# Performance work log

Measured on AMD Instinct MI355X. Metric: run time of the kernel, lower is better.

## Reference

```python
import jax, jax.numpy as jnp
import numpy as np

# Module hyperparameters (match init_kwargs)
C = 64      # in_channels
O = 256     # out_channels
K = 3       # filter_size
SUB = 2     # subsampling
SIGMA = 1.0
SCALE = 1.0 / SIGMA ** 2
EPS = 1e-8


def setup_inputs() -> dict:
    key = jax.random.key(0)
    k1, k2 = jax.random.split(key)
    x = jax.random.normal(k1, (32, C, 64, 64), dtype=jnp.float32)
    weight = jax.random.normal(k2, (O, C * K * K), dtype=jnp.float32)
    return {"x": x, "weight": weight}


def reference(x, weight):
    # Faithful to CKNLayer.forward, but expressed as a direct convolution
    # instead of materializing the im2col (unfold) tensor:
    #   unfold -> per-patch L2 norm -> (patches/norm) @ w_norm.T
    # == conv(x, w_norm) / patch_norm,   patch_norm = sqrt(conv(x^2, ones))
    B, _, H, W = x.shape
    pad = K // 2

    # F.normalize(weight, p=2, dim=1): clamp norm at 1e-12
    w_norm = weight / jnp.maximum(
        jnp.linalg.norm(weight, axis=1, keepdims=True), 1e-12
    )
    # torch unfold orders patch features as (c, kh, kw) -> reshape matches
    w4 = w_norm.reshape(O, C, K, K)

    dn = jax.lax.conv_dimension_numbers(x.shape, w4.shape, ('NCHW', 'OIHW', 'NCHW'))
    dots = jax.lax.conv_general_dilated(
        x, w4, window_strides=(1, 1), padding=[(pad, pad), (pad, pad)],
        dimension_numbers=dn)  # [B, O, H, W]

    ones_k = jnp.ones((1, C, K, K), x.dtype)
    sq = jax.lax.conv_general_dilated(
        x * x, ones_k, window_strides=(1, 1), padding=[(pad, pad), (pad, pad)],
        dimension_numbers=dn)  # [B, 1, H, W] = sum of squares per patch
    patch_norm = jnp.sqrt(jnp.maximum(sq, 0.0)) + EPS

    # Gaussian RBF on the unit sphere: exp(scale * (cos_sim - 1))
    out = jnp.exp(SCALE * (dots / patch_norm - 1.0))  # [B, O, H, W]

    # avg_pool2d(kernel=SUB, stride=SUB), H, W divisible by SUB
    out = out.reshape(B, O, H // SUB, SUB, W // SUB, SUB).mean(axis=(3, 5))
    return out
```

## Files before the change

### kernel.cpp

```cpp
#include <hip/hip_runtime.h>
#include <hip/hip_bf16.h>

typedef __attribute__((ext_vector_type(8))) short bf16x8;
typedef __attribute__((ext_vector_type(4))) float f32x4;
typedef __attribute__((ext_vector_type(16))) float f32x16;
typedef __attribute__((ext_vector_type(4))) unsigned u32x4;

__device__ __forceinline__ unsigned bfbits(float v) {
  __hip_bfloat16 h = __float2bfloat16(v);
  return (unsigned)*reinterpret_cast<unsigned short*>(&h);
}

__device__ __forceinline__ void wnorm_one(const float* __restrict__ w,
                                          ushort* __restrict__ wt,
                                          ushort* __restrict__ wt3,
                                          int o, int c) {
  float v[9];
  float ss = 0.f;
  const float* row = w + o * 576 + c * 9;
#pragma unroll
  for (int j = 0; j < 9; ++j) { v[j] = row[j]; ss += v[j] * v[j]; }
#pragma unroll
  for (int off = 32; off > 0; off >>= 1) ss += __shfl_xor(ss, off);
  const float inv = 1.0f / fmaxf(sqrtf(ss), 1e-12f);
  const int g = o >> 5, n = o & 31;
#pragma unroll
  for (int j = 0; j < 9; ++j) {
    const ushort bv = (ushort)bfbits(v[j] * inv);
    wt[o * 576 + j * 64 + c] = bv;
    const int ks = j * 4 + (c >> 4);
    wt3[((ks * 8 + g) * 32 + n) * 16 + (c & 15)] = bv;
  }
}

__global__ void wnorm_kernel(const float* __restrict__ w,
                             ushort* __restrict__ wt,
                             ushort* __restrict__ wt3) {
  wnorm_one(w, wt, wt3, blockIdx.x, threadIdx.x);
}

__global__ __launch_bounds__(256, 8) void xprep_kernel(
    const float* __restrict__ x, ushort* __restrict__ xt,
    float* __restrict__ css, const float* __restrict__ w,
    ushort* __restrict__ wt, ushort* __restrict__ wt3) {
  __shared__ __align__(16) unsigned tile[64 * 33];
  __shared__ __align__(16) float cssp[4 * 64];
  const int t = threadIdx.x;
  if (blockIdx.y == 32) {
    wnorm_one(w, wt, wt3, blockIdx.x * 4 + (t >> 6), t & 63);
    return;
  }
  const int y = blockIdx.x, b = blockIdx.y;
  const int c = t >> 2, m = t & 3;
  const int lane = t & 63, wv = t >> 6;

  const float* src = x + (((size_t)b * 64 + c) * 64 + y) * 64 + m * 4;
  float f[16];
#pragma unroll
  for (int j4 = 0; j4 < 4; ++j4) {
    const f32x4 v = *(const f32x4*)(src + j4 * 16);
#pragma unroll
    for (int k = 0; k < 4; ++k) f[j4 * 4 + k] = v[k];
  }
  float s[16];
#pragma unroll
  for (int j = 0; j < 16; ++j) {
    float v = f[j] * f[j];
    v += __shfl_xor(v, 4);
    v += __shfl_xor(v, 8);
    v += __shfl_xor(v, 16);
    v += __shfl_xor(v, 32);
    s[j] = v;
  }
  if (lane < 4) {
#pragma unroll
    for (int j4 = 0; j4 < 4; ++j4) {
      f32x4 v = {s[j4 * 4], s[j4 * 4 + 1], s[j4 * 4 + 2], s[j4 * 4 + 3]};
      *(f32x4*)(cssp + wv * 64 + j4 * 16 + lane * 4) = v;
    }
  }
  const int parity = c & 1;
  const int c2 = c >> 1;
#pragma unroll
  for (int j = 0; j < 16; ++j) {
    const float pf = __shfl_xor(f[j], 4);
    const bool mine = parity ? (j >= 8) : (j < 8);
    if (mine) {
      const unsigned dw = parity ? (bfbits(pf) | (bfbits(f[j]) << 16))
                                 : (bfbits(f[j]) | (bfbits(pf) << 16));
      const int px = (j >> 2) * 16 + m * 4 + (j & 3);
      tile[px * 33 + c2] = dw;
    }
  }
  __syncthreads();
  {
    const int xr = t >> 2, q = t & 3;
    unsigned d[8];
#pragma unroll
    for (int i = 0; i < 8; ++i) d[i] = tile[xr * 33 + q * 8 + i];
    ushort* dst = xt + (((size_t)b * 64 + y) * 64 + xr) * 64 + q * 16;
    u32x4 v0 = {d[0], d[1], d[2], d[3]};
    u32x4 v1 = {d[4], d[5], d[6], d[7]};
    *(u32x4*)dst = v0;
    *(u32x4*)(dst + 8) = v1;
  }
  if (t < 64) {
    const float sum = cssp[t] + cssp[64 + t] + cssp[128 + t] + cssp[192 + t];
    css[((size_t)b * 64 + y) * 64 + t] = sum;
  }
}

__global__ __launch_bounds__(512, 4) void ckn_main(
    const ushort* __restrict__ xt, const float* __restrict__ css,
    const ushort* __restrict__ wt3, float* __restrict__ out) {
  __shared__ __align__(16) char smem[67328];
  char* const xs = smem;
  float* const pool = (float*)(smem + 33792);
  float* const invp = (float*)(smem + 66816);
  const int PS = 258;

  const int tid = threadIdx.x;
  const int y0 = blockIdx.x;
  const int b = blockIdx.y;

  if (tid < 128) {
    const int ry = tid >> 6, xx = tid & 63;
    const int yc = 2 * y0 + ry;
    float s = 0.f;
#pragma unroll
    for (int dy = -1; dy <= 1; ++dy) {
      const int yy = yc + dy;
      if ((unsigned)yy < 64u) s += css[((size_t)b * 64 + yy) * 64 + xx];
    }
    const float sl = __shfl_up(s, 1);
    const float sr = __shfl_down(s, 1);
    const float tot = s + ((xx > 0) ? sl : 0.f) + ((xx < 63) ? sr : 0.f);
    invp[tid] = 1.0f / (sqrtf(fmaxf(tot, 0.f)) + 1e-8f);
  }

  if (tid < 64) {
    const int r4 = tid >> 4, colsel = (tid >> 3) & 1, cblk = tid & 7;
    *(f32x4*)(xs + r4 * 8448 + colsel * 65 * 128 + cblk * 16) =
        (f32x4){0.f, 0.f, 0.f, 0.f};
  }

  {
    const int xx = tid >> 3;
    const int c0 = 8 * ((tid & 7) ^ ((xx + 1) & 7));
    const ushort* srcb = xt + ((size_t)b * 64) * 4096 + (size_t)xx * 64 + c0;
#pragma unroll
    for (int r4 = 0; r4 < 4; ++r4) {
      const int y_img = 2 * y0 - 1 + r4;
      char* dst = xs + r4 * 8448 + 128 + tid * 16;
      if ((unsigned)y_img < 64u) {
        const ushort* src = srcb + (size_t)y_img * 4096;
        __builtin_amdgcn_global_load_lds(
            (const __attribute__((address_space(1))) void*)src,
            (__attribute__((address_space(3))) void*)dst, 16, 0, 0);
      } else {
        *(f32x4*)dst = (f32x4){0.f, 0.f, 0.f, 0.f};
      }
    }
  }

  const int lane = tid & 63;
  const int wid = tid >> 6;
  const int wave_m = wid & 1;
  const int wave_n = wid >> 1;
  const int lane31 = lane & 31;
  const int hi = lane >> 5;

  const ushort* wb3 = wt3 + (size_t)lane31 * 16 + hi * 8;
  const int g0 = wave_n * 2;

  bf16x8 bq[2][2];
#pragma unroll
  for (int nf = 0; nf < 2; ++nf) {
    bq[0][nf] = *(const bf16x8*)(wb3 + (size_t)(0 * 8 + g0 + nf) * 512);
    bq[1][nf] = *(const bf16x8*)(wb3 + (size_t)(1 * 8 + g0 + nf) * 512);
  }

  const int hi16 = hi << 4;
  int PH[2][3];
#pragma unroll
  for (int mf = 0; mf < 2; ++mf)
#pragma unroll
    for (int kw = 0; kw < 3; ++kw) {
      const int col = mf * 32 + lane31 + kw;
      PH[mf][kw] = (col * 128 + ((col & 7) << 4)) ^ hi16;
    }
  const int rb0 = wave_m * 8448;

  __syncthreads();

  f32x16 acc[2][2];
#pragma unroll
  for (int i = 0; i < 2; ++i)
#pragma unroll
    for (int j = 0; j < 2; ++j)
#pragma unroll
      for (int e = 0; e < 16; ++e) acc[i][j][e] = 0.f;

#pragma unroll
  for (int ks = 0; ks < 36; ++ks) {
    const int t9 = ks >> 2;
    const int kh = t9 / 3, kw = t9 % 3;
    const int ksc = (ks & 3) << 5;
    const int cur = ks & 1;
    bf16x8 afrag[2];
#pragma unroll
    for (int mf = 0; mf < 2; ++mf)
      afrag[mf] = *(const bf16x8*)(xs + rb0 + kh * 8448 + (PH[mf][kw] ^ ksc));
    __builtin_amdgcn_s_setprio(1);
#pragma unroll
    for (int mf = 0; mf < 2; ++mf)
#pragma unroll
      for (int nf = 0; nf < 2; ++nf)
        acc[mf][nf] = __builtin_amdgcn_mfma_f32_32x32x16_bf16(
            afrag[mf], bq[cur][nf], acc[mf][nf], 0, 0, 0);
    __builtin_amdgcn_s_setprio(0);
    if (ks + 2 < 36) {
#pragma unroll
      for (int nf = 0; nf < 2; ++nf)
        bq[cur][nf] =
            *(const bf16x8*)(wb3 + (size_t)((ks + 2) * 8 + g0 + nf) * 512);
    }
  }

  if (wave_m == 1) {
#pragma unroll
    for (int mf = 0; mf < 2; ++mf)
#pragma unroll
      for (int q = 0; q < 4; ++q) {
        const f32x4 ip = *(const f32x4*)(invp + 64 + mf * 32 + 8 * q + 4 * hi);
        const int px = mf * 16 + 4 * q + 2 * hi;
#pragma unroll
        for (int nf = 0; nf < 2; ++nf) {
          const int o = wave_n * 64 + nf * 32 + lane31;
          const float e0 = __expf(acc[mf][nf][4 * q + 0] * ip[0] - 1.f);
          const float e1 = __expf(acc[mf][nf][4 * q + 1] * ip[1] - 1.f);
          const float e2 = __expf(acc[mf][nf][4 * q + 2] * ip[2] - 1.f);
          const float e3 = __expf(acc[mf][nf][4 * q + 3] * ip[3] - 1.f);
          pool[px * PS + o] = e0 + e1;
          pool[(px + 1) * PS + o] = e2 + e3;
        }
      }
  }
  __syncthreads();
  if (wave_m == 0) {
#pragma unroll
    for (int mf = 0; mf < 2; ++mf)
#pragma unroll
      for (int q = 0; q < 4; ++q) {
        const f32x4 ip = *(const f32x4*)(invp + mf * 32 + 8 * q + 4 * hi);
        const int px = mf * 16 + 4 * q + 2 * hi;
#pragma unroll
        for (int nf = 0; nf < 2; ++nf) {
          const int o = wave_n * 64 + nf * 32 + lane31;
          const float e0 = __expf(acc[mf][nf][4 * q + 0] * ip[0] - 1.f);
          const float e1 = __expf(acc[mf][nf][4 * q + 1] * ip[1] - 1.f);
          const float e2 = __expf(acc[mf][nf][4 * q + 2] * ip[2] - 1.f);
          const float e3 = __expf(acc[mf][nf][4 * q + 3] * ip[3] - 1.f);
          pool[px * PS + o] = 0.25f * (pool[px * PS + o] + e0 + e1);
          pool[(px + 1) * PS + o] = 0.25f * (pool[(px + 1) * PS + o] + e2 + e3);
        }
      }
  }
  __syncthreads();

  const size_t obase = (((size_t)b * 256) * 32 + y0) * 32;
#pragma unroll
  for (int j = 0; j < 4; ++j) {
    const int o = j * 64 + (tid >> 3);
    const int ch = (tid & 7) * 4;
    const f32x4 v = {pool[(ch + 0) * PS + o], pool[(ch + 1) * PS + o],
                     pool[(ch + 2) * PS + o], pool[(ch + 3) * PS + o]};
    *(f32x4*)(out + obase + (size_t)o * 1024 + ch) = v;
  }
}

__global__ __launch_bounds__(512, 4) void ckn_main_v1(
    const float* __restrict__ x, const ushort* __restrict__ wt,
    float* __restrict__ out) {
  __shared__ __align__(16) char smem[43552];
  char* const xs = smem;
  float* const invp = (float*)(smem + 33792);
  float* const cs = (float*)(smem + 34304);
  float* const csp = (float*)(smem + 35360);
  float* const pool = (float*)smem;

  const int tid = threadIdx.x;
  const int y0 = blockIdx.x;
  const int b = blockIdx.y;

  if (tid < 64) {
    const int r4 = tid >> 4, colsel = (tid >> 3) & 1, cblk = tid & 7;
    const int col = colsel * 65;
    *(f32x4*)(xs + r4 * 8448 + col * 128 + cblk * 16) =
        (f32x4){0.f, 0.f, 0.f, 0.f};
  }
  {
    const int xx = tid & 63;
    const int cg = tid >> 6;
    const int col = xx + 1;
    const int sw = (cg * 16) ^ ((col & 7) << 4);
#pragma unroll
    for (int r4 = 0; r4 < 4; ++r4) {
      const int y_img = 2 * y0 - 1 + r4;
      char* dst = xs + r4 * 8448 + col * 128 + sw;
      if ((unsigned)y_img < 64u) {
        const float* src =
            x + (((size_t)b * 64 + cg * 8) * 64 + y_img) * 64 + xx;
        float ss = 0.f;
        union { bf16x8 v; ushort u[8]; } pk;
#pragma unroll
        for (int j = 0; j < 8; ++j) {
          const float f = src[(size_t)j * 4096];
          ss += f * f;
          pk.u[j] = (ushort)bfbits(f);
        }
        *(bf16x8*)dst = pk.v;
        csp[(r4 * 8 + cg) * 64 + xx] = ss;
      } else {
        *(bf16x8*)dst = (bf16x8){0, 0, 0, 0, 0, 0, 0, 0};
        csp[(r4 * 8 + cg) * 64 + xx] = 0.f;
      }
    }
  }
  __syncthreads();
  if (tid < 256) {
    const int r4 = tid >> 6, xc = tid & 63;
    float s = 0.f;
#pragma unroll
    for (int cg = 0; cg < 8; ++cg) s += csp[(r4 * 8 + cg) * 64 + xc];
    cs[r4 * 66 + xc + 1] = s;
  }
  if (tid >= 256 && tid < 264) {
    const int t = tid - 256;
    cs[(t >> 1) * 66 + (t & 1) * 65] = 0.f;
  }
  __syncthreads();
  if (tid < 128) {
    const int ry = tid >> 6, xp = tid & 63;
    float s = 0.f;
#pragma unroll
    for (int dr = 0; dr < 3; ++dr)
#pragma unroll
      for (int dc = 0; dc < 3; ++dc) s += cs[(ry + dr) * 66 + xp + dc];
    invp[tid] = 1.0f / (sqrtf(fmaxf(s, 0.f)) + 1e-8f);
  }
  __syncthreads();

  const int lane = tid & 63;
  const int wid = tid >> 6;
  const int wave_m = wid & 1;
  const int wave_n = wid >> 1;
  const int lane16 = lane & 15;
  const int klane = lane >> 4;
  const int o_base = wave_n * 64;

  f32x4 acc[4][4];
#pragma unroll
  for (int i = 0; i < 4; ++i)
#pragma unroll
    for (int j = 0; j < 4; ++j) acc[i][j] = (f32x4){0.f, 0.f, 0.f, 0.f};
  const ushort* wbase = wt + (o_base + lane16) * 576 + klane * 8;
#pragma unroll
  for (int ks = 0; ks < 18; ++ks) {
    const int t9 = ks >> 1;
    const int kh = t9 / 3, kw = t9 % 3;
    const int cb = (ks & 1) * 64 + klane * 16;
    bf16x8 bfrag[4];
#pragma unroll
    for (int fn = 0; fn < 4; ++fn)
      bfrag[fn] = *(const bf16x8*)(wbase + fn * 16 * 576 + ks * 32);
    const int r4 = wave_m + kh;
#pragma unroll
    for (int fm = 0; fm < 4; ++fm) {
      const int col = fm * 16 + lane16 + kw;
      const int addr = r4 * 8448 + col * 128 + (cb ^ ((col & 7) << 4));
      const bf16x8 afrag = *(const bf16x8*)(xs + addr);
#pragma unroll
      for (int fn = 0; fn < 4; ++fn)
        acc[fm][fn] = __builtin_amdgcn_mfma_f32_16x16x32_bf16(
            afrag, bfrag[fn], acc[fm][fn], 0, 0, 0);
    }
  }
  float ep0[4][4], ep1[4][4];
#pragma unroll
  for (int fm = 0; fm < 4; ++fm) {
    const int m = wave_m * 64 + fm * 16 + klane * 4;
    const f32x4 ip = *(const f32x4*)(invp + m);
#pragma unroll
    for (int fn = 0; fn < 4; ++fn) {
      const f32x4 v = acc[fm][fn];
      const float e0 = __expf(v[0] * ip[0] - 1.f);
      const float e1 = __expf(v[1] * ip[1] - 1.f);
      const float e2 = __expf(v[2] * ip[2] - 1.f);
      const float e3 = __expf(v[3] * ip[3] - 1.f);
      ep0[fm][fn] = e0 + e1;
      ep1[fm][fn] = e2 + e3;
    }
  }
  __syncthreads();
  if (wave_m == 1) {
#pragma unroll
    for (int fm = 0; fm < 4; ++fm) {
      const int ox = fm * 8 + klane * 2;
#pragma unroll
      for (int fn = 0; fn < 4; ++fn) {
        const int o = o_base + fn * 16 + lane16;
        *(float2*)(pool + o * 32 + ox) = make_float2(ep0[fm][fn], ep1[fm][fn]);
      }
    }
  }
  __syncthreads();
  if (wave_m == 0) {
#pragma unroll
    for (int fm = 0; fm < 4; ++fm) {
      const int ox = fm * 8 + klane * 2;
#pragma unroll
      for (int fn = 0; fn < 4; ++fn) {
        const int o = o_base + fn * 16 + lane16;
        const float2 othr = *(const float2*)(pool + o * 32 + ox);
        const float r0 = 0.25f * (ep0[fm][fn] + othr.x);
        const float r1 = 0.25f * (ep1[fm][fn] + othr.y);
        *(float2*)(out + ((((size_t)b * 256 + o) * 32 + y0) * 32 + ox)) =
            make_float2(r0, r1);
      }
    }
  }
}

extern "C" void kernel_launch(void* const* d_in, const int* in_sizes, int n_in,
                              void* d_out, int out_size, void* d_ws,
                              size_t ws_size, hipStream_t stream) {
  const float* x = (const float*)d_in[0];
  const float* w = (const float*)d_in[1];
  float* out = (float*)d_out;

  const size_t XT_BYTES = 32ull * 64 * 64 * 64 * 2;
  const size_t CSS_BYTES = 32ull * 64 * 64 * 4;
  const size_t WT_BYTES = 256ull * 576 * 2;
  const size_t NEED = XT_BYTES + CSS_BYTES + 2 * WT_BYTES;

  if (ws_size >= NEED) {
    ushort* xt = (ushort*)d_ws;
    float* css = (float*)((char*)d_ws + XT_BYTES);
    ushort* wt = (ushort*)((char*)d_ws + XT_BYTES + CSS_BYTES);
    ushort* wt3 = (ushort*)((char*)d_ws + XT_BYTES + CSS_BYTES + WT_BYTES);

    xprep_kernel<<<dim3(64, 33), dim3(256), 0, stream>>>(x, xt, css, w, wt,
                                                         wt3);
    ckn_main<<<dim3(32, 32), dim3(512), 0, stream>>>(xt, css, wt3, out);
  } else {
    ushort* wt = (ushort*)d_ws;
    ushort* wt3 = wt + 256 * 576;
    if (ws_size >= 2 * WT_BYTES) {
      wnorm_kernel<<<dim3(256), dim3(64), 0, stream>>>(w, wt, wt3);
      ckn_main_v1<<<dim3(32, 32), dim3(512), 0, stream>>>(x, wt, out);
    }
  }
}
```

Before: 64.26 us.

## Store transposed input channel-block-major and use padded LDS rows instead of XOR swizzle

```diff
diff --git a/kernel.cpp b/kernel.cpp
--- a/kernel.cpp
+++ b/kernel.cpp
@@ -94,15 +94,16 @@
   }
   __syncthreads();
   {
-    const int xr = t >> 2, q = t & 3;
+    const int xr = t & 63, q = t >> 6;
     unsigned d[8];
 #pragma unroll
     for (int i = 0; i < 8; ++i) d[i] = tile[xr * 33 + q * 8 + i];
-    ushort* dst = xt + (((size_t)b * 64 + y) * 64 + xr) * 64 + q * 16;
+    ushort* dst =
+        xt + ((((size_t)b * 64 + y) * 8 + 2 * q) * 64 + xr) * 8;
     u32x4 v0 = {d[0], d[1], d[2], d[3]};
     u32x4 v1 = {d[4], d[5], d[6], d[7]};
     *(u32x4*)dst = v0;
-    *(u32x4*)(dst + 8) = v1;
+    *(u32x4*)(dst + 512) = v1;
   }
   if (t < 64) {
     const float sum = cssp[t] + cssp[64 + t] + cssp[128 + t] + cssp[192 + t];
@@ -139,19 +140,19 @@
   }
 
   if (tid < 64) {
-    const int r4 = tid >> 4, colsel = (tid >> 3) & 1, cblk = tid & 7;
-    *(f32x4*)(xs + r4 * 8448 + colsel * 65 * 128 + cblk * 16) =
+    const int r4 = tid >> 4, cb = (tid >> 1) & 7, colsel = tid & 1;
+    *(f32x4*)(xs + r4 * 8448 + cb * 1056 + colsel * 65 * 16) =
         (f32x4){0.f, 0.f, 0.f, 0.f};
   }
 
   {
-    const int xx = tid >> 3;
-    const int c0 = 8 * ((tid & 7) ^ ((xx + 1) & 7));
-    const ushort* srcb = xt + ((size_t)b * 64) * 4096 + (size_t)xx * 64 + c0;
+    const int l = tid & 63;
+    const int w = tid >> 6;
+    const ushort* srcb = xt + (((size_t)b * 64) * 8 + w) * 512 + l * 8;
 #pragma unroll
     for (int r4 = 0; r4 < 4; ++r4) {
       const int y_img = 2 * y0 - 1 + r4;
-      char* dst = xs + r4 * 8448 + 128 + tid * 16;
+      char* dst = xs + r4 * 8448 + w * 1056 + (l + 1) * 16;
       if ((unsigned)y_img < 64u) {
         const ushort* src = srcb + (size_t)y_img * 4096;
         __builtin_amdgcn_global_load_lds(
@@ -180,16 +181,13 @@
     bq[1][nf] = *(const bf16x8*)(wb3 + (size_t)(1 * 8 + g0 + nf) * 512);
   }
 
-  const int hi16 = hi << 4;
   int PH[2][3];
 #pragma unroll
   for (int mf = 0; mf < 2; ++mf)
 #pragma unroll
-    for (int kw = 0; kw < 3; ++kw) {
-      const int col = mf * 32 + lane31 + kw;
-      PH[mf][kw] = (col * 128 + ((col & 7) << 4)) ^ hi16;
-    }
-  const int rb0 = wave_m * 8448;
+    for (int kw = 0; kw < 3; ++kw)
+      PH[mf][kw] =
+          (mf * 32 + lane31 + kw) * 16 + hi * 1056 + wave_m * 8448;
 
   __syncthreads();
 
@@ -205,12 +203,12 @@
   for (int ks = 0; ks < 36; ++ks) {
     const int t9 = ks >> 2;
     const int kh = t9 / 3, kw = t9 % 3;
-    const int ksc = (ks & 3) << 5;
+    const int stepoff = kh * 8448 + (ks & 3) * 2112;
     const int cur = ks & 1;
     bf16x8 afrag[2];
 #pragma unroll
     for (int mf = 0; mf < 2; ++mf)
-      afrag[mf] = *(const bf16x8*)(xs + rb0 + kh * 8448 + (PH[mf][kw] ^ ksc));
+      afrag[mf] = *(const bf16x8*)(xs + PH[mf][kw] + stepoff);
     __builtin_amdgcn_s_setprio(1);
 #pragma unroll
     for (int mf = 0; mf < 2; ++mf)
```

Result: no change. 64.43 us (+0.3%).
